# Optimization experiments

Measured on AMD Instinct MI355X. Metric: run time of the kernel, lower is better.

The kernel has to match this reference:

```python
import jax, jax.numpy as jnp
import numpy as np
import math

N, C_IN, H, W = 8, 64, 128, 128
C_OUT, K = 128, 5
MU = 0.9

def _masks():
    _mu = (1.0 - MU) / 3.0
    neighbor = jnp.array([
        [0, _mu, 0, _mu, 0],
        [_mu, _mu, _mu, _mu, _mu],
        [0, _mu, 0, _mu, 0],
        [_mu, _mu, _mu, _mu, _mu],
        [0, _mu, 0, _mu, 0]], dtype=jnp.float32)
    dilator = jnp.array([
        [1.0, 0.0, 1.0, 0.0, 1.0],
        [0.0, 0.0, 0.0, 0.0, 0.0],
        [1.0, 0.0, 1.0, 0.0, 1.0],
        [0.0, 0.0, 0.0, 0.0, 0.0],
        [1.0, 0.0, 1.0, 0.0, 1.0]], dtype=jnp.float32)
    return neighbor, dilator

def setup_inputs() -> dict:
    key = jax.random.key(0)
    k1, k2 = jax.random.split(key)
    input_ = jax.random.normal(k1, (N, C_IN, H, W), dtype=jnp.float32)
    stdv = 1.0 / math.sqrt(C_IN * K * K)
    weight = jax.random.uniform(k2, (C_OUT, C_IN, K, K), dtype=jnp.float32,
                                minval=-stdv, maxval=stdv)
    return {"input_": input_, "weight": weight}

def reference(input_, weight):
    # Faithful math: f_kernel = weight * dilator_mask + neighbor_weight_mask,
    # then a standard 5x5 conv (stride=1, pad=2, dilation=1). The original
    # realizes the conv via F.unfold + matmul (im2col); conv_general_dilated
    # computes identical values. Bias exists as a parameter but is never
    # applied in the original forward, so it is omitted here.
    neighbor, dilator = _masks()
    f_kernel = weight * dilator + neighbor  # broadcast over (O, I)
    out = jax.lax.conv_general_dilated(
        input_, f_kernel,
        window_strides=(1, 1),
        padding=((2, 2), (2, 2)),
        rhs_dilation=(1, 1),
        dimension_numbers=("NCHW", "OIHW", "NCHW"))
    return out  # [N, C_OUT, H, W]
```

## Files before the change

kernel.cpp:

```cpp
#include <hip/hip_runtime.h>

typedef short short8 __attribute__((ext_vector_type(8)));
typedef float f32x4 __attribute__((ext_vector_type(4)));

#define NN 8
#define CI 64
#define CO 128
#define HH 128
#define WW 128
#define PH 132
#define PW 132
#define MU 0.033333333333333333f

#define WS_W_BYTES (9 * 128 * 64 * 2)
#define WS_T_OFF   WS_W_BYTES
#define WS_T_BYTES (NN * PH * PW * 4)
#define WS_X_OFF   (WS_T_OFF + WS_T_BYTES)
#define WS_X_BYTES ((size_t)NN * PH * PW * CI * 2)
#define WS_NB_OFF  (WS_X_OFF + WS_X_BYTES)
#define WS_TOTAL   (WS_NB_OFF + WS_T_BYTES)

__device__ __forceinline__ unsigned short f2bf(float f) {
  unsigned u = __float_as_uint(f);
  u += 0x7fffu + ((u >> 16) & 1u);
  return (unsigned short)(u >> 16);
}

__device__ __forceinline__ void g2lds16(const void* g, void* l) {
  __builtin_amdgcn_global_load_lds(
      (const __attribute__((address_space(1))) unsigned int*)g,
      (__attribute__((address_space(3))) unsigned int*)l, 16, 0, 0);
}
__device__ __forceinline__ void g2lds4(const void* g, void* l) {
  __builtin_amdgcn_global_load_lds(
      (const __attribute__((address_space(1))) unsigned int*)g,
      (__attribute__((address_space(3))) unsigned int*)l, 4, 0, 0);
}

__global__ __launch_bounds__(256) void prep_kernel(
    const float* __restrict__ in, const float* __restrict__ w,
    unsigned short* __restrict__ ws_w, float* __restrict__ ws_T,
    short8* __restrict__ ws_x) {
  const int b = blockIdx.x, tid = threadIdx.x;
  if (b < 512) {
    __shared__ short8 lx[256][8];
    const int n = b >> 6, pair = b & 63;
    const int px = tid;
    const int r = pair * 2 + (px >> 7), x = px & 127;
    const float* src = in + ((size_t)(n * CI) * HH + r) * WW + x;
    float tsum = 0.f;
    #pragma unroll
    for (int g = 0; g < 8; ++g) {
      short8 pk;
      #pragma unroll
      for (int j = 0; j < 8; ++j) {
        const float v = src[(size_t)(g * 8 + j) * (HH * WW)];
        tsum += v;
        pk[j] = (short)f2bf(v);
      }
      lx[px][g ^ (px & 7)] = pk;
    }
    ws_T[(n * PH + r + 2) * PW + (x + 2)] = tsum;
    __syncthreads();
    #pragma unroll
    for (int it = 0; it < 8; ++it) {
      const int G = it * 256 + tid;
      const int px2 = G >> 3, g2 = G & 7;
      const int r2 = pair * 2 + (px2 >> 7), x2 = px2 & 127;
      ws_x[((size_t)(n * PH + r2 + 2) * PW + (x2 + 2)) * 8 + g2] =
          lx[px2][g2 ^ (px2 & 7)];
    }
  } else if (b < 520) {
    const int n = b - 512;
    const short8 z = {0, 0, 0, 0, 0, 0, 0, 0};
    for (int e = tid; e < 1040 * 8; e += 256) {
      const int px = e >> 3, g = e & 7;
      int y, x;
      if (px < 528) { const int r4 = px / 132; y = (r4 < 2) ? r4 : r4 + 128; x = px - r4 * 132; }
      else { const int q = px - 528; const int c4 = q >> 7; x = (c4 < 2) ? c4 : c4 + 128; y = 2 + (q & 127); }
      ws_x[((size_t)(n * PH + y) * PW + x) * 8 + g] = z;
    }
    for (int e = tid; e < 1040; e += 256) {
      int y, x;
      if (e < 528) { const int r4 = e / 132; y = (r4 < 2) ? r4 : r4 + 128; x = e - r4 * 132; }
      else { const int q = e - 528; const int c4 = q >> 7; x = (c4 < 2) ? c4 : c4 + 128; y = 2 + (q & 127); }
      ws_T[(n * PH + y) * PW + x] = 0.f;
    }
  } else {
    const int el = (b - 520) * 256 + tid;
    const int lane = el & 63;
    const int idx = el >> 6;
    const int ks = idx & 1, cb = (idx >> 1) & 7, tap = idx >> 4;
    const int lo = lane & 15, hi = lane >> 4;
    const int ky = (tap / 3) * 2, kx = (tap % 3) * 2;
    const float* wp = w + (size_t)((cb * 16 + lo) * 64 + ks * 32 + hi * 8) * 25
                        + ky * 5 + kx;
    short8 pk;
    #pragma unroll
    for (int j = 0; j < 8; ++j) pk[j] = (short)f2bf(wp[j * 25]);
    ((short8*)ws_w)[el] = pk;
  }
}

__global__ __launch_bounds__(256) void nb_kernel(
    const float* __restrict__ ws_T, float* __restrict__ ws_nb) {
  const int p = blockIdx.x * 256 + threadIdx.x;
  const int n = p >> 14, yx = p & 16383;
  const int y = yx >> 7, x = yx & 127;
  const float* Tb = ws_T + (size_t)(n * PH + y) * PW + x;
  float s = 0.f;
  #pragma unroll
  for (int ky = 0; ky < 5; ++ky)
    #pragma unroll
    for (int kx = 0; kx < 5; ++kx)
      if ((ky & 1) | (kx & 1)) s += Tb[ky * PW + kx];
  ws_nb[(size_t)p] = s * MU;
}

__global__ __launch_bounds__(256)
__attribute__((amdgpu_waves_per_eu(2, 2)))
void conv_kernel(
    const unsigned short* __restrict__ ws_w, const float* __restrict__ ws_nb,
    const unsigned short* __restrict__ ws_x, float* __restrict__ out) {
  __shared__ short8 halo[288 * 8];
  __shared__ float  nbt[128];

  const int tid = threadIdx.x;
  const int wave = tid >> 6, lane = tid & 63;
  const int bid = blockIdx.x;
  const int n = bid & 7;
  const int rest = bid >> 3;
  const int cob = rest & 3;
  const int ty0 = (rest >> 2) * 4;
  const int lo = lane & 15, hi = lane >> 4;

  const short8* wsv = (const short8*)ws_w;
  short8 W[36];
  #pragma unroll
  for (int k = 0; k < 36; ++k)
    W[k] = wsv[((k >> 2) * 16 + cob * 4 + (k & 3)) * 64 + lane];

  for (int j = 0; j < 4; ++j) {
    const int tx0 = j * 32;

    for (int k = wave; k < 36; k += 4) {
      const int pos = k * 8 + (lane >> 3);
      const int r = pos / 36, c = pos - r * 36;
      const int chunk = (lane & 7) ^ (pos & 7);
      const unsigned short* g =
          ws_x + ((size_t)(n * PH + ty0 + r) * PW + (tx0 + c)) * 64 + chunk * 8;
      g2lds16(g, (char*)halo + k * 1024);
    }
    if (wave < 2) {
      const float* g = ws_nb
          + (size_t)((n * 128 + ty0 + 2 * wave + (lane >> 5)) * 128)
          + tx0 + (lane & 31);
      g2lds4(g, (char*)nbt + wave * 256);
    }
    __syncthreads();

    const f32x4 nbv0 = *(const f32x4*)&nbt[wave * 32 + 0  + hi * 4];
    const f32x4 nbv1 = *(const f32x4*)&nbt[wave * 32 + 16 + hi * 4];
    f32x4 acc00 = nbv0, acc01 = nbv1;
    f32x4 acc10 = nbv0, acc11 = nbv1;

    short8 Aaf0, Aaf1;
    short8 Baf0, Baf1;
    short8 Caf0, Caf1;

#define LOADSET(P, K) { \
      constexpr int tap_ = (K) >> 1, ks_ = (K) & 1; \
      constexpr int ty_ = (tap_ / 3) * 2, tx_ = (tap_ % 3) * 2; \
      const int p0_ = (wave + ty_) * 36 + (lo + tx_); \
      const int p1_ = p0_ + 16; \
      P##af0 = halo[p0_ * 8 + ((ks_ * 4 + hi) ^ (p0_ & 7))]; \
      P##af1 = halo[p1_ * 8 + ((ks_ * 4 + hi) ^ (p1_ & 7))]; \
    }
#define MFMASET(P, K) { \
      constexpr int tap_ = (K) >> 1, ks_ = (K) & 1; \
      acc00 = __builtin_amdgcn_mfma_f32_16x16x32_bf16(P##af0, W[tap_ * 4 + 0 + ks_], acc00, 0, 0, 0); \
      acc01 = __builtin_amdgcn_mfma_f32_16x16x32_bf16(P##af1, W[tap_ * 4 + 0 + ks_], acc01, 0, 0, 0); \
      acc10 = __builtin_amdgcn_mfma_f32_16x16x32_bf16(P##af0, W[tap_ * 4 + 2 + ks_], acc10, 0, 0, 0); \
      acc11 = __builtin_amdgcn_mfma_f32_16x16x32_bf16(P##af1, W[tap_ * 4 + 2 + ks_], acc11, 0, 0, 0); \
    }

    LOADSET(A, 0); LOADSET(B, 1);
    LOADSET(C, 2);  MFMASET(A, 0);
    LOADSET(A, 3);  MFMASET(B, 1);
    LOADSET(B, 4);  MFMASET(C, 2);
    LOADSET(C, 5);  MFMASET(A, 3);
    LOADSET(A, 6);  MFMASET(B, 4);
    LOADSET(B, 7);  MFMASET(C, 5);
    LOADSET(C, 8);  MFMASET(A, 6);
    LOADSET(A, 9);  MFMASET(B, 7);
    LOADSET(B, 10); MFMASET(C, 8);
    LOADSET(C, 11); MFMASET(A, 9);
    LOADSET(A, 12); MFMASET(B, 10);
    LOADSET(B, 13); MFMASET(C, 11);
    LOADSET(C, 14); MFMASET(A, 12);
    LOADSET(A, 15); MFMASET(B, 13);
    LOADSET(B, 16); MFMASET(C, 14);
    LOADSET(C, 17); MFMASET(A, 15);
    MFMASET(B, 16);
    MFMASET(C, 17);
#undef LOADSET
#undef MFMASET

    {
      const int gy = ty0 + wave;
      const int gx0 = tx0 + hi * 4;
      const int co0 = cob * 32 + lo;
      *(f32x4*)&out[(((size_t)n * CO + co0) * HH + gy) * WW + gx0] = acc00;
      *(f32x4*)&out[(((size_t)n * CO + co0) * HH + gy) * WW + gx0 + 16] = acc01;
      *(f32x4*)&out[(((size_t)n * CO + co0 + 16) * HH + gy) * WW + gx0] = acc10;
      *(f32x4*)&out[(((size_t)n * CO + co0 + 16) * HH + gy) * WW + gx0 + 16] = acc11;
    }
    __syncthreads();
  }
}

__global__ __launch_bounds__(256) void prep_kernel_safe(
    const float* __restrict__ in, const float* __restrict__ w,
    unsigned short* __restrict__ ws_w, float* __restrict__ ws_T) {
  const int bid = blockIdx.x, tid = threadIdx.x;
  if (bid < 288) {
    const int el = bid * 256 + tid;
    const int tap = el >> 13;
    const int rem = el & 8191;
    const int co = rem >> 6, ic = rem & 63;
    const int ky = (tap / 3) * 2, kx = (tap % 3) * 2;
    ws_w[el] = f2bf(w[(co * 64 + ic) * 25 + ky * 5 + kx]);
  } else {
    const int p = (bid - 288) * 256 + tid;
    const int n = p >> 14;
    const int yx = p & 16383;
    const float* base = in + (size_t)n * CI * (HH * WW) + yx;
    float s = 0.f;
    #pragma unroll
    for (int ic = 0; ic < CI; ++ic) s += base[ic * (HH * WW)];
    ws_T[p] = s;
  }
}

#define SHR 12
#define SHC 36
#define SNPOS (SHR * SHC)

__global__ __launch_bounds__(256, 2) void conv_kernel_safe(
    const float* __restrict__ in, const unsigned short* __restrict__ ws_w,
    const float* __restrict__ ws_T, float* __restrict__ out) {
  __shared__ short8 in_lds[SNPOS * 8];
  __shared__ float T_lds[SNPOS];

  const int tid = threadIdx.x;
  const int t = blockIdx.x;
  const int n = blockIdx.y;
  const int ty0 = (t >> 2) * 8;
  const int tx0 = (t & 3) * 32;

  for (int e = tid; e < SNPOS * 8; e += 256) {
    const int slot = e / SNPOS;
    const int pos = e - slot * SNPOS;
    const int r = pos / SHC, c = pos - r * SHC;
    const int gy = ty0 + r - 2, gx = tx0 + c - 2;
    const bool ok = (gy >= 0 && gy < HH && gx >= 0 && gx < WW);
    const long off = ((long)(n * CI + slot * 8) * HH + gy) * WW + gx;
    short8 pk;
    #pragma unroll
    for (int j = 0; j < 8; ++j) {
      const float v = ok ? in[off + (long)j * (HH * WW)] : 0.f;
      pk[j] = (short)f2bf(v);
    }
    in_lds[pos * 8 + (slot ^ (pos & 7))] = pk;
  }
  for (int e = tid; e < SNPOS; e += 256) {
    const int r = e / SHC, c = e - r * SHC;
    const int gy = ty0 + r - 2, gx = tx0 + c - 2;
    T_lds[e] = (gy >= 0 && gy < HH && gx >= 0 && gx < WW)
                   ? ws_T[((size_t)n * HH + gy) * WW + gx] : 0.f;
  }
  __syncthreads();

  const int wave = tid >> 6;
  const int lane = tid & 63;
  const int lo = lane & 15;
  const int hi = lane >> 4;

  int py[4], pxc[4];
  #pragma unroll
  for (int f = 0; f < 4; ++f) {
    const int pb = wave * 64 + f * 16;
    py[f] = pb >> 5;
    pxc[f] = (pb & 31) + lo;
  }

  f32x4 acc[8][4];
  #pragma unroll
  for (int cb = 0; cb < 8; ++cb)
    #pragma unroll
    for (int f = 0; f < 4; ++f) acc[cb][f] = (f32x4){0.f, 0.f, 0.f, 0.f};

  const short8* wsv = (const short8*)ws_w;

  #pragma unroll
  for (int tap = 0; tap < 9; ++tap) {
    const int ty = (tap / 3) * 2, tx = (tap % 3) * 2;
    #pragma unroll
    for (int ks = 0; ks < 2; ++ks) {
      short8 bfrag[4];
      #pragma unroll
      for (int f = 0; f < 4; ++f) {
        const int pos = (py[f] + ty) * SHC + (pxc[f] + tx);
        bfrag[f] = in_lds[pos * 8 + ((ks * 4 + hi) ^ (pos & 7))];
      }
      #pragma unroll
      for (int cb = 0; cb < 8; ++cb) {
        const short8 afrag = wsv[(tap * 128 + cb * 16 + lo) * 8 + ks * 4 + hi];
        #pragma unroll
        for (int f = 0; f < 4; ++f)
          acc[cb][f] = __builtin_amdgcn_mfma_f32_16x16x32_bf16(
              afrag, bfrag[f], acc[cb][f], 0, 0, 0);
      }
    }
  }

  float nb[4];
  #pragma unroll
  for (int f = 0; f < 4; ++f) {
    float s = 0.f;
    #pragma unroll
    for (int ky = 0; ky < 5; ++ky)
      #pragma unroll
      for (int kx = 0; kx < 5; ++kx)
        if ((ky & 1) | (kx & 1))
          s += T_lds[(py[f] + ky) * SHC + (pxc[f] + kx)];
    nb[f] = s * MU;
  }

  #pragma unroll
  for (int cb = 0; cb < 8; ++cb) {
    #pragma unroll
    for (int f = 0; f < 4; ++f) {
      const int gy = ty0 + py[f];
      const int gx = tx0 + pxc[f];
      #pragma unroll
      for (int q = 0; q < 4; ++q) {
        const int co = cb * 16 + hi * 4 + q;
        out[(((size_t)n * CO + co) * HH + gy) * WW + gx] = acc[cb][f][q] + nb[f];
      }
    }
  }
}

extern "C" void kernel_launch(void* const* d_in, const int* in_sizes, int n_in,
                              void* d_out, int out_size, void* d_ws, size_t ws_size,
                              hipStream_t stream) {
  const float* in = (const float*)d_in[0];
  const float* w  = (const float*)d_in[1];
  float* out = (float*)d_out;
  unsigned short* ws_w = (unsigned short*)d_ws;

  if (ws_size >= WS_TOTAL) {
    float* ws_T = (float*)((char*)d_ws + WS_T_OFF);
    short8* ws_x = (short8*)((char*)d_ws + WS_X_OFF);
    float* ws_nb = (float*)((char*)d_ws + WS_NB_OFF);
    prep_kernel<<<dim3(556), 256, 0, stream>>>(in, w, ws_w, ws_T, ws_x);
    nb_kernel<<<dim3(512), 256, 0, stream>>>(ws_T, ws_nb);
    conv_kernel<<<dim3(1024), 256, 0, stream>>>(
        ws_w, ws_nb, (const unsigned short*)ws_x, out);
  } else {
    float* ws_T = (float*)((char*)d_ws + WS_W_BYTES);
    prep_kernel_safe<<<dim3(288 + 512), 256, 0, stream>>>(in, w, ws_w, ws_T);
    conv_kernel_safe<<<dim3(64, NN), 256, 0, stream>>>(in, ws_w, ws_T, out);
  }
}
```

Before: 45.01 us.

## Double-buffer halo and neighbor tiles in LDS to overlap loads with MFMA

The conv kernel now keeps two LDS buffers for the input halo and the neighbor-bias tile. It prefetches the next 32-column unit while MFMAs run on the current one, using a partial vmcnt wait and a single barrier per iteration. Idle waves issue dummy loads so every wave has the same outstanding-load count, which keeps the vmcnt(4) wait uniform. This doubles LDS use, which may lower occupancy, and the correctness of the wait count depends on the exact number of loads each wave issues.

```diff
diff --git a/kernel.cpp b/kernel.cpp
--- a/kernel.cpp
+++ b/kernel.cpp
@@ -122,8 +122,9 @@
 void conv_kernel(
     const unsigned short* __restrict__ ws_w, const float* __restrict__ ws_nb,
     const unsigned short* __restrict__ ws_x, float* __restrict__ out) {
-  __shared__ short8 halo[288 * 8];
-  __shared__ float  nbt[128];
+  __shared__ short8 halo[2][288 * 8];
+  __shared__ float  nbt[2][128];
+  __shared__ float  dmy[128];
 
   const int tid = threadIdx.x;
   const int wave = tid >> 6, lane = tid & 63;
@@ -140,27 +141,43 @@
   for (int k = 0; k < 36; ++k)
     W[k] = wsv[((k >> 2) * 16 + cob * 4 + (k & 3)) * 64 + lane];
 
-  for (int j = 0; j < 4; ++j) {
-    const int tx0 = j * 32;
-
+  auto issue_unit = [&](int tx0, int b) {
     for (int k = wave; k < 36; k += 4) {
       const int pos = k * 8 + (lane >> 3);
       const int r = pos / 36, c = pos - r * 36;
       const int chunk = (lane & 7) ^ (pos & 7);
       const unsigned short* g =
           ws_x + ((size_t)(n * PH + ty0 + r) * PW + (tx0 + c)) * 64 + chunk * 8;
-      g2lds16(g, (char*)halo + k * 1024);
+      g2lds16(g, (char*)halo[b] + k * 1024);
     }
     if (wave < 2) {
       const float* g = ws_nb
           + (size_t)((n * 128 + ty0 + 2 * wave + (lane >> 5)) * 128)
           + tx0 + (lane & 31);
-      g2lds4(g, (char*)nbt + wave * 256);
-    }
-    __syncthreads();
-
-    const f32x4 nbv0 = *(const f32x4*)&nbt[wave * 32 + 0  + hi * 4];
-    const f32x4 nbv1 = *(const f32x4*)&nbt[wave * 32 + 16 + hi * 4];
+      g2lds4(g, (char*)nbt[b] + wave * 256);
+    } else {
+      const float* g = ws_nb
+          + (size_t)((n * 128 + ty0 + (lane >> 5)) * 128) + (lane & 31);
+      g2lds4(g, (char*)dmy + (wave - 2) * 256);
+    }
+  };
+
+  issue_unit(0, 0);
+
+  for (int j = 0; j < 4; ++j) {
+    const int tx0 = j * 32;
+    const int cur = j & 1;
+
+    if (j == 0) { asm volatile("s_waitcnt vmcnt(0)" ::: "memory"); }
+    else        { asm volatile("s_waitcnt vmcnt(4)" ::: "memory"); }
+    __builtin_amdgcn_sched_barrier(0);
+    __builtin_amdgcn_s_barrier();
+    __builtin_amdgcn_sched_barrier(0);
+
+    if (j < 3) issue_unit(tx0 + 32, cur ^ 1);
+
+    const f32x4 nbv0 = *(const f32x4*)&nbt[cur][wave * 32 + 0  + hi * 4];
+    const f32x4 nbv1 = *(const f32x4*)&nbt[cur][wave * 32 + 16 + hi * 4];
     f32x4 acc00 = nbv0, acc01 = nbv1;
     f32x4 acc10 = nbv0, acc11 = nbv1;
 
@@ -173,8 +190,8 @@
       constexpr int ty_ = (tap_ / 3) * 2, tx_ = (tap_ % 3) * 2; \
       const int p0_ = (wave + ty_) * 36 + (lo + tx_); \
       const int p1_ = p0_ + 16; \
-      P##af0 = halo[p0_ * 8 + ((ks_ * 4 + hi) ^ (p0_ & 7))]; \
-      P##af1 = halo[p1_ * 8 + ((ks_ * 4 + hi) ^ (p1_ & 7))]; \
+      P##af0 = halo[cur][p0_ * 8 + ((ks_ * 4 + hi) ^ (p0_ & 7))]; \
+      P##af1 = halo[cur][p1_ * 8 + ((ks_ * 4 + hi) ^ (p1_ & 7))]; \
     }
 #define MFMASET(P, K) { \
       constexpr int tap_ = (K) >> 1, ks_ = (K) & 1; \
@@ -215,7 +232,6 @@
       *(f32x4*)&out[(((size_t)n * CO + co0 + 16) * HH + gy) * WW + gx0] = acc10;
       *(f32x4*)&out[(((size_t)n * CO + co0 + 16) * HH + gy) * WW + gx0 + 16] = acc11;
     }
-    __syncthreads();
   }
 }
 
```

Result: slower. 46.10 us (+2.4%).
